# Kernel optimization log

Hardware: AMD Instinct MI355X
Metric: run time of the kernel (lower is better)

## Reference

```python
import jax, jax.numpy as jnp
import numpy as np

ALPHA = 0.2  # LeakyReLU negative slope


def setup_inputs() -> dict:
    key = jax.random.key(0)
    k1, k2, k3 = jax.random.split(key, 3)
    B, N, D_in, D_out = 16, 2048, 128, 128
    x = jax.random.normal(k1, (B, N, D_in), dtype=jnp.float32)
    # xavier-uniform-ish scale for params
    W = jax.random.normal(k2, (D_in, D_out), dtype=jnp.float32) * (1.414 / np.sqrt(D_in + D_out))
    a = jax.random.normal(k3, (2 * D_out, 1), dtype=jnp.float32) * (1.414 / np.sqrt(2 * D_out + 1))
    return {"x": x, "W": W, "a": a}


def reference(x, W, a):
    # h: (B, N, D)
    h = jnp.matmul(x, W)
    D = h.shape[-1]
    # a = [a1; a2]; e[b,i,j] = leakyrelu(a1 . h_i + a2 . h_j)
    a1 = a[:D, 0]   # (D,)
    a2 = a[D:, 0]   # (D,)
    s1 = jnp.einsum('bnd,d->bn', h, a1)  # (B, N) source term
    s2 = jnp.einsum('bnd,d->bn', h, a2)  # (B, N) target term
    e = jax.nn.leaky_relu(s1[:, :, None] + s2[:, None, :], negative_slope=ALPHA)  # (B, N, N)
    attention = jax.nn.softmax(e, axis=2)
    h_prime = jnp.matmul(attention, h)  # (B, N, D)
    return jax.nn.relu(h_prime)  # concat=True -> relu
```

## Files before the change

### kernel.cpp

```cpp
#include <hip/hip_runtime.h>
#include <hip/hip_bf16.h>
#include <cstddef>

#define GAT_B 16
#define GAT_N 2048
#define GAT_D 128
#define GAT_ROWS (GAT_B * GAT_N)
#define CH 256
#define CL 8
#define GAT_ALPHA 0.2f

typedef __attribute__((ext_vector_type(8))) short short8v;
typedef __attribute__((ext_vector_type(4))) float f32x4;

__device__ __forceinline__ void cvt_hilo(float x, unsigned short& hi, unsigned short& lo) {
  union { float f; unsigned u; } a;
  a.f = x;
  hi = (unsigned short)(a.u >> 16);
  union { unsigned u; float f; } b;
  b.u = (unsigned)hi << 16;
  union { float f; unsigned u; } c;
  c.f = x - b.f;
  lo = (unsigned short)(c.u >> 16);
}

__global__ __launch_bounds__(256) void k1_gemm(const float* __restrict__ x,
                                               const float* __restrict__ W,
                                               const float* __restrict__ aa,
                                               float* __restrict__ h,
                                               float* __restrict__ s1part,
                                               float* __restrict__ s2part) {
  __shared__ unsigned short xH[64 * 128];
  __shared__ unsigned short xL[64 * 128];
  const int tid = threadIdx.x;
  const int row0 = blockIdx.x * 64;

#pragma unroll
  for (int p = 0; p < 8; ++p) {
    const int row = p * 8 + (tid >> 5);
    const int f4 = tid & 31;
    const float4 v = ((const float4*)(x + (size_t)(row0 + row) * GAT_D))[f4];
    unsigned short h0, h1, h2, h3, l0, l1, l2, l3;
    cvt_hilo(v.x, h0, l0);
    cvt_hilo(v.y, h1, l1);
    cvt_hilo(v.z, h2, l2);
    cvt_hilo(v.w, h3, l3);
    const int slot = (f4 >> 1) ^ (row & 7);
    const int base = row * 128 + slot * 8 + (f4 & 1) * 4;
    *(ushort4*)&xH[base] = make_ushort4(h0, h1, h2, h3);
    *(ushort4*)&xL[base] = make_ushort4(l0, l1, l2, l3);
  }

  const int w = tid >> 6, l = tid & 63;
  const int wc0 = w * 32;
  const int g = l >> 4, c16 = l & 15;

  short8v bh[4][2], bl[4][2];
#pragma unroll
  for (int ks = 0; ks < 4; ++ks)
#pragma unroll
    for (int nt = 0; nt < 2; ++nt) {
      const int n = wc0 + nt * 16 + c16;
#pragma unroll
      for (int j = 0; j < 8; ++j) {
        unsigned short hi, lo;
        cvt_hilo(W[(ks * 32 + g * 8 + j) * 128 + n], hi, lo);
        bh[ks][nt][j] = (short)hi;
        bl[ks][nt][j] = (short)lo;
      }
    }

  __syncthreads();

  f32x4 acc[4][2];
#pragma unroll
  for (int mt = 0; mt < 4; ++mt)
#pragma unroll
    for (int nt = 0; nt < 2; ++nt) acc[mt][nt] = (f32x4)(0.f);

#pragma unroll
  for (int ks = 0; ks < 4; ++ks) {
    short8v ah[4], al[4];
#pragma unroll
    for (int mt = 0; mt < 4; ++mt) {
      const int row = mt * 16 + c16;
      const int ai = row * 128 + (((ks * 4 + g) ^ (row & 7)) * 8);
      ah[mt] = *(const short8v*)&xH[ai];
      al[mt] = *(const short8v*)&xL[ai];
    }
#pragma unroll
    for (int mt = 0; mt < 4; ++mt) {
#pragma unroll
      for (int nt = 0; nt < 2; ++nt) {
        acc[mt][nt] = __builtin_amdgcn_mfma_f32_16x16x32_bf16(ah[mt], bh[ks][nt], acc[mt][nt], 0, 0, 0);
        acc[mt][nt] = __builtin_amdgcn_mfma_f32_16x16x32_bf16(al[mt], bh[ks][nt], acc[mt][nt], 0, 0, 0);
        acc[mt][nt] = __builtin_amdgcn_mfma_f32_16x16x32_bf16(ah[mt], bl[ks][nt], acc[mt][nt], 0, 0, 0);
      }
    }
  }

#pragma unroll
  for (int mt = 0; mt < 4; ++mt)
#pragma unroll
    for (int nt = 0; nt < 2; ++nt)
#pragma unroll
      for (int j = 0; j < 4; ++j)
        h[(size_t)(row0 + mt * 16 + g * 4 + j) * GAT_D + wc0 + nt * 16 + c16] =
            acc[mt][nt][j];

  float a1v[2], a2v[2];
#pragma unroll
  for (int nt = 0; nt < 2; ++nt) {
    a1v[nt] = aa[wc0 + nt * 16 + c16];
    a2v[nt] = aa[128 + wc0 + nt * 16 + c16];
  }
#pragma unroll
  for (int mt = 0; mt < 4; ++mt) {
#pragma unroll
    for (int j = 0; j < 4; ++j) {
      float t1 = acc[mt][0][j] * a1v[0] + acc[mt][1][j] * a1v[1];
      float t2 = acc[mt][0][j] * a2v[0] + acc[mt][1][j] * a2v[1];
#pragma unroll
      for (int off = 1; off < 16; off <<= 1) {
        t1 += __shfl_xor(t1, off);
        t2 += __shfl_xor(t2, off);
      }
      if (c16 == 0) {
        const int row = row0 + mt * 16 + g * 4 + j;
        s1part[w * GAT_ROWS + row] = t1;
        s2part[w * GAT_ROWS + row] = t2;
      }
    }
  }
}

__global__ __launch_bounds__(1024) void k2_sort(const float* __restrict__ s1part,
                                                const float* __restrict__ s2part,
                                                float* __restrict__ s2s,
                                                int* __restrict__ idxs,
                                                float* __restrict__ s1s,
                                                int* __restrict__ rids,
                                                float* __restrict__ wA,
                                                float* __restrict__ wP,
                                                float* __restrict__ preDenA,
                                                float* __restrict__ sufDenP) {
  __shared__ float v[2048];
  __shared__ int id[2048];
  __shared__ float wtotA[16];
  __shared__ float wtotP[16];
  const int tid = threadIdx.x;
  const int b = blockIdx.x >> 1;
  const int half = blockIdx.x & 1;
  const int i0 = tid, i1 = tid + 1024;
  const float* src = (half == 0) ? s2part : s1part;
  {
    const int r0 = b * GAT_N + i0, r1 = b * GAT_N + i1;
    float v0 = src[r0] + src[GAT_ROWS + r0] + src[2 * GAT_ROWS + r0] + src[3 * GAT_ROWS + r0];
    float v1 = src[r1] + src[GAT_ROWS + r1] + src[2 * GAT_ROWS + r1] + src[3 * GAT_ROWS + r1];
    if (half == 1) {
      v0 = -v0;
      v1 = -v1;
    }
    v[i0] = v0;
    v[i1] = v1;
  }
  __syncthreads();

  const int lane = tid & 63;
  const int e0 = ((tid >> 6) << 7) + lane * 2;
  const int e1 = e0 + 1;
  float va = v[e0], vb = v[e1];
  int ida = e0, idb = e1;

  auto lanex = [&](int k, int j) {
    const int jl = j >> 1;
    const bool dir = (e0 & k) == 0;
    const bool lower = (lane & jl) == 0;
    const bool keepMax = lower ^ dir;
    {
      const float ov = __shfl_xor(va, jl);
      const int oid = __shfl_xor(ida, jl);
      const bool ogt = (ov > va) || (ov == va && oid > ida);
      if (ogt == keepMax) { va = ov; ida = oid; }
    }
    {
      const float ov = __shfl_xor(vb, jl);
      const int oid = __shfl_xor(idb, jl);
      const bool ogt = (ov > vb) || (ov == vb && oid > idb);
      if (ogt == keepMax) { vb = ov; idb = oid; }
    }
  };
  auto pairx = [&](int k) {
    const bool dir = (e0 & k) == 0;
    const bool bgt = (vb > va) || (vb == va && idb > ida);
    if (bgt != dir) {
      const float tv = va; va = vb; vb = tv;
      const int ti = ida; ida = idb; idb = ti;
    }
  };

#pragma unroll
  for (int k = 2; k <= 128; k <<= 1) {
#pragma unroll
    for (int j = k >> 1; j >= 2; j >>= 1) lanex(k, j);
    pairx(k);
  }
  v[e0] = va; id[e0] = ida;
  v[e1] = vb; id[e1] = idb;
  __syncthreads();

  for (int k = 256; k <= 2048; k <<= 1) {
    for (int j = k >> 1; j >= 128; j >>= 1) {
      const int i = ((tid & ~(j - 1)) << 1) | (tid & (j - 1));
      const int ixj = i | j;
      const bool up = (i & k) == 0;
      const float x0 = v[i], x1 = v[ixj];
      if (up ? (x0 > x1) : (x0 < x1)) {
        v[i] = x1;
        v[ixj] = x0;
        const int ti = id[i];
        id[i] = id[ixj];
        id[ixj] = ti;
      }
      __syncthreads();
    }
    va = v[e0]; ida = id[e0];
    vb = v[e1]; idb = id[e1];
#pragma unroll
    for (int j = 64; j >= 2; j >>= 1) lanex(k, j);
    pairx(k);
    v[e0] = va; id[e0] = ida;
    v[e1] = vb; id[e1] = idb;
    __syncthreads();
  }

  if (half == 1) {
    s1s[b * GAT_N + i0] = -v[i0];
    s1s[b * GAT_N + i1] = -v[i1];
    rids[b * GAT_N + i0] = id[i0];
    rids[b * GAT_N + i1] = id[i1];
    return;
  }
  s2s[b * GAT_N + i0] = v[i0];
  s2s[b * GAT_N + i1] = v[i1];
  idxs[b * GAT_N + i0] = id[i0];
  idxs[b * GAT_N + i1] = id[i1];

  const int w = tid >> 6;
  const float aL = __expf(GAT_ALPHA * v[2 * tid]);
  const float aR = __expf(GAT_ALPHA * v[2 * tid + 1]);
  const float pL = __expf(v[2047 - 2 * tid]);
  const float pR = __expf(v[2046 - 2 * tid]);
  wA[b * GAT_N + 2 * tid] = aL;
  wA[b * GAT_N + 2 * tid + 1] = aR;
  wP[b * GAT_N + 2047 - 2 * tid] = pL;
  wP[b * GAT_N + 2046 - 2 * tid] = pR;
  float sA = aL + aR, sP = pL + pR;
#pragma unroll
  for (int off = 1; off < 64; off <<= 1) {
    const float tA = __shfl_up(sA, off);
    const float tP = __shfl_up(sP, off);
    if (lane >= off) {
      sA += tA;
      sP += tP;
    }
  }
  if (lane == 63) {
    wtotA[w] = sA;
    wtotP[w] = sP;
  }
  __syncthreads();
  float offA = 0.f, offP = 0.f;
  for (int ww = 0; ww < w; ++ww) {
    offA += wtotA[ww];
    offP += wtotP[ww];
  }
  const float inclA = offA + sA;
  const float inclP = offP + sP;
  preDenA[b * GAT_N + 2 * tid] = inclA - aR;
  preDenA[b * GAT_N + 2 * tid + 1] = inclA;
  sufDenP[b * GAT_N + 2047 - 2 * tid] = inclP - pR;
  sufDenP[b * GAT_N + 2046 - 2 * tid] = inclP;
}

__global__ __launch_bounds__(128) void k3_permute(const float* __restrict__ h,
                                                  const int* __restrict__ idxs,
                                                  const float* __restrict__ wA,
                                                  const float* __restrict__ wP,
                                                  float* __restrict__ hs,
                                                  float* __restrict__ partA,
                                                  float* __restrict__ partP) {
  const int b = blockIdx.x >> 7, cc = blockIdx.x & 127;
  const int d = threadIdx.x;
  const int* idxb = idxs + b * GAT_N;
  const float* hb = h + (size_t)b * GAT_N * GAT_D;
#pragma unroll
  for (int sub = 0; sub < 2; ++sub) {
    const int c = cc * 2 + sub;
    const int q0 = c * CL;
    float accA = 0.f, accP = 0.f;
#pragma unroll
    for (int qq = 0; qq < CL; ++qq) {
      const int q = q0 + qq;
      const int j = idxb[q];
      const float hv = hb[(size_t)j * GAT_D + d];
      hs[((size_t)b * GAT_N + q) * GAT_D + d] = hv;
      accA = fmaf(wA[b * GAT_N + q], hv, accA);
      accP = fmaf(wP[b * GAT_N + q], hv, accP);
    }
    partA[(b * CH + c) * GAT_D + d] = accA;
    partP[(b * CH + c) * GAT_D + d] = accP;
  }
}

__global__ __launch_bounds__(1024) void k3b_prep(const float* __restrict__ s1s,
                                                 const float* __restrict__ s2s,
                                                 const float* __restrict__ preDenA,
                                                 const float* __restrict__ sufDenP,
                                                 const float* __restrict__ partA,
                                                 const float* __restrict__ partP,
                                                 float* __restrict__ baseA,
                                                 float* __restrict__ baseP,
                                                 int* __restrict__ pArr,
                                                 float* __restrict__ c1,
                                                 float* __restrict__ c2) {
  __shared__ float totA[8][128];
  __shared__ float totP[8][128];
  __shared__ float sh[2048];
  const int b = blockIdx.x >> 1;
  const int role = blockIdx.x & 1;
  const int t = threadIdx.x;
  if (role == 0) {
    const int d = t & 127, g = t >> 7;
    const float* pA = partA + (size_t)(b * CH + g * 32) * GAT_D + d;
    const float* pP = partP + (size_t)(b * CH + g * 32) * GAT_D + d;
    float sA = 0.f, sP = 0.f;
#pragma unroll 8
    for (int i = 0; i < 32; ++i) {
      sA += pA[i * GAT_D];
      sP += pP[i * GAT_D];
    }
    totA[g][d] = sA;
    totP[g][d] = sP;
    __syncthreads();
    float offA = 0.f, offP = 0.f;
    for (int gg = 0; gg < g; ++gg) offA += totA[gg][d];
    for (int gg = g + 1; gg < 8; ++gg) offP += totP[gg][d];
    float run = offA;
#pragma unroll 8
    for (int i = 0; i < 32; ++i) {
      baseA[(size_t)(b * (CH + 1) + g * 32 + i) * GAT_D + d] = run;
      run += pA[i * GAT_D];
    }
    if (g == 7) baseA[(size_t)(b * (CH + 1) + CH) * GAT_D + d] = run;
    run = offP;
#pragma unroll 8
    for (int i = 31; i >= 0; --i) {
      baseP[(size_t)(b * CH + g * 32 + i) * GAT_D + d] = run;
      run += pP[i * GAT_D];
    }
  } else {
    sh[t] = s2s[b * GAT_N + t];
    sh[t + 1024] = s2s[b * GAT_N + t + 1024];
    __syncthreads();
#pragma unroll
    for (int rr = 0; rr < 2; ++rr) {
      const int j = t + rr * 1024;
      const float s1v = s1s[b * GAT_N + j];
      const float tt = -s1v;
      int lo = 0, hi = GAT_N;
      while (lo < hi) {
        const int mid = (lo + hi) >> 1;
        if (sh[mid] < tt)
          lo = mid + 1;
        else
          hi = mid;
      }
      const float e1 = __expf(s1v), e2 = __expf(GAT_ALPHA * s1v);
      float den = 0.f;
      if (lo < GAT_N) den += e1 * sufDenP[b * GAT_N + lo];
      if (lo > 0) den += e2 * preDenA[b * GAT_N + lo - 1];
      const float inv = 1.f / den;
      pArr[b * GAT_N + j] = lo;
      c1[b * GAT_N + j] = e1 * inv;
      c2[b * GAT_N + j] = e2 * inv;
    }
  }
}

__global__ __launch_bounds__(256) void k5_out(const float* __restrict__ hs,
                                              const float* __restrict__ wA,
                                              const float* __restrict__ wP,
                                              const float* __restrict__ baseA,
                                              const float* __restrict__ baseP,
                                              const int* __restrict__ pArr,
                                              const float* __restrict__ c1,
                                              const float* __restrict__ c2,
                                              const int* __restrict__ rids,
                                              float* __restrict__ out) {
  const int wave = threadIdx.x >> 6, lane = threadIdx.x & 63;
  const int j = blockIdx.x * 4 + wave;
  const int b = j >> 11;
  const int jr = b * GAT_N + (j & 2047);
  const int p = pArr[jr];
  const float cc1 = c1[jr], cc2 = c2[jr];
  const int rid = rids[jr];
  const float2* hs2 = (const float2*)(hs + (size_t)b * GAT_N * GAT_D);
  const float* wAb = wA + b * GAT_N;
  const float* wPb = wP + b * GAT_N;

  const int cA = p >> 3;
  float2 accA = ((const float2*)(baseA + (size_t)(b * (CH + 1) + cA) * GAT_D))[lane];
#pragma unroll 4
  for (int q = cA * CL; q < p; ++q) {
    const float w = wAb[q];
    const float2 hv = hs2[(size_t)q * 64 + lane];
    accA.x = fmaf(w, hv.x, accA.x);
    accA.y = fmaf(w, hv.y, accA.y);
  }

  const int pP = p < GAT_N ? p : GAT_N - 1;
  const int cP = pP >> 3;
  float2 accP = ((const float2*)(baseP + (size_t)(b * CH + cP) * GAT_D))[lane];
  const int qend = cP * CL + CL;
#pragma unroll 4
  for (int q = p; q < qend; ++q) {
    const float w = wPb[q];
    const float2 hv = hs2[(size_t)q * 64 + lane];
    accP.x = fmaf(w, hv.x, accP.x);
    accP.y = fmaf(w, hv.y, accP.y);
  }

  const float vx = cc2 * accA.x + cc1 * accP.x;
  const float vy = cc2 * accA.y + cc1 * accP.y;
  ((float2*)out)[(size_t)(b * GAT_N + rid) * 64 + lane] =
      make_float2(fmaxf(vx, 0.f), fmaxf(vy, 0.f));
}

extern "C" void kernel_launch(void* const* d_in, const int* in_sizes, int n_in,
                              void* d_out, int out_size, void* d_ws, size_t ws_size,
                              hipStream_t stream) {
  (void)in_sizes;
  (void)n_in;
  (void)out_size;
  (void)ws_size;
  const float* x = (const float*)d_in[0];
  const float* W = (const float*)d_in[1];
  const float* a = (const float*)d_in[2];
  float* out = (float*)d_out;
  float* wsf = (float*)d_ws;

  const size_t HN = (size_t)GAT_ROWS * GAT_D;
  size_t o = 0;
  float* s1part = wsf + o;   o += 4 * GAT_ROWS;
  float* s2part = wsf + o;   o += 4 * GAT_ROWS;
  float* s2s = wsf + o;      o += GAT_ROWS;
  int* idxs = (int*)(wsf + o); o += GAT_ROWS;
  float* s1s = wsf + o;      o += GAT_ROWS;
  int* rids = (int*)(wsf + o); o += GAT_ROWS;
  float* preDenA = wsf + o;  o += GAT_ROWS;
  float* sufDenP = wsf + o;  o += GAT_ROWS;
  float* wAr = wsf + o;      o += GAT_ROWS;
  float* wPr = wsf + o;      o += GAT_ROWS;
  int* pArr = (int*)(wsf + o); o += GAT_ROWS;
  float* c1 = wsf + o;       o += GAT_ROWS;
  float* c2 = wsf + o;       o += GAT_ROWS;
  float* partA = wsf + o;    o += (size_t)GAT_B * CH * GAT_D;
  float* partP = wsf + o;    o += (size_t)GAT_B * CH * GAT_D;
  float* baseA = wsf + o;    o += (size_t)GAT_B * (CH + 1) * GAT_D;
  float* baseP = wsf + o;    o += (size_t)GAT_B * CH * GAT_D;
  float* h = wsf + o;        o += HN;
  float* hs = wsf + o;       o += HN;

  k1_gemm<<<512, 256, 0, stream>>>(x, W, a, h, s1part, s2part);
  k2_sort<<<2 * GAT_B, 1024, 0, stream>>>(s1part, s2part, s2s, idxs, s1s, rids, wAr, wPr,
                                          preDenA, sufDenP);
  k3_permute<<<GAT_B * 128, 128, 0, stream>>>(h, idxs, wAr, wPr, hs, partA, partP);
  k3b_prep<<<2 * GAT_B, 1024, 0, stream>>>(s1s, s2s, preDenA, sufDenP, partA, partP,
                                           baseA, baseP, pArr, c1, c2);
  k5_out<<<GAT_ROWS / 4, 256, 0, stream>>>(hs, wAr, wPr, baseA, baseP, pArr, c1, c2,
                                           rids, out);
}
```

Before: 66.35 us.

## Move binary search and softmax coefficients into sort kernel, slim scan kernel

The per-row binary search and softmax-denominator coefficient computation move from the prep kernel into the s2-sort block. That block now keeps prefix/suffix denominators in shared memory and indexes results by natural row id instead of sorted order. The prep kernel is reduced to the partial-sum scan over half as many blocks. Several intermediate global arrays (s1s, s2s, preDenA, sufDenP) go away. The output kernel now gathers p/c1/c2 through rids and uses 512-thread blocks, while the sort block takes on extra serial work.

```diff
diff --git a/kernel.cpp b/kernel.cpp
--- a/kernel.cpp
+++ b/kernel.cpp
@@ -136,16 +136,17 @@
 
 __global__ __launch_bounds__(1024) void k2_sort(const float* __restrict__ s1part,
                                                 const float* __restrict__ s2part,
-                                                float* __restrict__ s2s,
                                                 int* __restrict__ idxs,
-                                                float* __restrict__ s1s,
                                                 int* __restrict__ rids,
                                                 float* __restrict__ wA,
                                                 float* __restrict__ wP,
-                                                float* __restrict__ preDenA,
-                                                float* __restrict__ sufDenP) {
+                                                int* __restrict__ pNat,
+                                                float* __restrict__ c1,
+                                                float* __restrict__ c2) {
   __shared__ float v[2048];
   __shared__ int id[2048];
+  __shared__ float denA[2048];
+  __shared__ float denP[2048];
   __shared__ float wtotA[16];
   __shared__ float wtotP[16];
   const int tid = threadIdx.x;
@@ -235,14 +236,10 @@
   }
 
   if (half == 1) {
-    s1s[b * GAT_N + i0] = -v[i0];
-    s1s[b * GAT_N + i1] = -v[i1];
     rids[b * GAT_N + i0] = id[i0];
     rids[b * GAT_N + i1] = id[i1];
     return;
   }
-  s2s[b * GAT_N + i0] = v[i0];
-  s2s[b * GAT_N + i1] = v[i1];
   idxs[b * GAT_N + i0] = id[i0];
   idxs[b * GAT_N + i1] = id[i1];
 
@@ -277,10 +274,36 @@
   }
   const float inclA = offA + sA;
   const float inclP = offP + sP;
-  preDenA[b * GAT_N + 2 * tid] = inclA - aR;
-  preDenA[b * GAT_N + 2 * tid + 1] = inclA;
-  sufDenP[b * GAT_N + 2047 - 2 * tid] = inclP - pR;
-  sufDenP[b * GAT_N + 2046 - 2 * tid] = inclP;
+  denA[2 * tid] = inclA - aR;
+  denA[2 * tid + 1] = inclA;
+  denP[2047 - 2 * tid] = inclP - pR;
+  denP[2046 - 2 * tid] = inclP;
+  __syncthreads();
+
+#pragma unroll
+  for (int rr = 0; rr < 2; ++rr) {
+    const int j = tid + rr * 1024;
+    const int r = b * GAT_N + j;
+    const float s1v = s1part[r] + s1part[GAT_ROWS + r] + s1part[2 * GAT_ROWS + r] +
+                      s1part[3 * GAT_ROWS + r];
+    const float tt = -s1v;
+    int lo = 0, hi = GAT_N;
+    while (lo < hi) {
+      const int mid = (lo + hi) >> 1;
+      if (v[mid] < tt)
+        lo = mid + 1;
+      else
+        hi = mid;
+    }
+    const float e1 = __expf(s1v), e2 = __expf(GAT_ALPHA * s1v);
+    float den = 0.f;
+    if (lo < GAT_N) den += e1 * denP[lo];
+    if (lo > 0) den += e2 * denA[lo - 1];
+    const float inv = 1.f / den;
+    pNat[r] = lo;
+    c1[r] = e1 * inv;
+    c2[r] = e2 * inv;
+  }
 }
 
 __global__ __launch_bounds__(128) void k3_permute(const float* __restrict__ h,
@@ -313,98 +336,62 @@
   }
 }
 
-__global__ __launch_bounds__(1024) void k3b_prep(const float* __restrict__ s1s,
-                                                 const float* __restrict__ s2s,
-                                                 const float* __restrict__ preDenA,
-                                                 const float* __restrict__ sufDenP,
-                                                 const float* __restrict__ partA,
+__global__ __launch_bounds__(1024) void k3b_scan(const float* __restrict__ partA,
                                                  const float* __restrict__ partP,
                                                  float* __restrict__ baseA,
-                                                 float* __restrict__ baseP,
-                                                 int* __restrict__ pArr,
-                                                 float* __restrict__ c1,
-                                                 float* __restrict__ c2) {
+                                                 float* __restrict__ baseP) {
   __shared__ float totA[8][128];
   __shared__ float totP[8][128];
-  __shared__ float sh[2048];
-  const int b = blockIdx.x >> 1;
-  const int role = blockIdx.x & 1;
+  const int b = blockIdx.x;
   const int t = threadIdx.x;
-  if (role == 0) {
-    const int d = t & 127, g = t >> 7;
-    const float* pA = partA + (size_t)(b * CH + g * 32) * GAT_D + d;
-    const float* pP = partP + (size_t)(b * CH + g * 32) * GAT_D + d;
-    float sA = 0.f, sP = 0.f;
+  const int d = t & 127, g = t >> 7;
+  const float* pA = partA + (size_t)(b * CH + g * 32) * GAT_D + d;
+  const float* pP = partP + (size_t)(b * CH + g * 32) * GAT_D + d;
+  float sA = 0.f, sP = 0.f;
 #pragma unroll 8
-    for (int i = 0; i < 32; ++i) {
-      sA += pA[i * GAT_D];
-      sP += pP[i * GAT_D];
-    }
-    totA[g][d] = sA;
-    totP[g][d] = sP;
-    __syncthreads();
-    float offA = 0.f, offP = 0.f;
-    for (int gg = 0; gg < g; ++gg) offA += totA[gg][d];
-    for (int gg = g + 1; gg < 8; ++gg) offP += totP[gg][d];
-    float run = offA;
+  for (int i = 0; i < 32; ++i) {
+    sA += pA[i * GAT_D];
+    sP += pP[i * GAT_D];
+  }
+  totA[g][d] = sA;
+  totP[g][d] = sP;
+  __syncthreads();
+  float offA = 0.f, offP = 0.f;
+  for (int gg = 0; gg < g; ++gg) offA += totA[gg][d];
+  for (int gg = g + 1; gg < 8; ++gg) offP += totP[gg][d];
+  float run = offA;
 #pragma unroll 8
-    for (int i = 0; i < 32; ++i) {
-      baseA[(size_t)(b * (CH + 1) + g * 32 + i) * GAT_D + d] = run;
-      run += pA[i * GAT_D];
-    }
-    if (g == 7) baseA[(size_t)(b * (CH + 1) + CH) * GAT_D + d] = run;
-    run = offP;
+  for (int i = 0; i < 32; ++i) {
+    baseA[(size_t)(b * (CH + 1) + g * 32 + i) * GAT_D + d] = run;
+    run += pA[i * GAT_D];
+  }
+  if (g == 7) baseA[(size_t)(b * (CH + 1) + CH) * GAT_D + d] = run;
+  run = offP;
 #pragma unroll 8
-    for (int i = 31; i >= 0; --i) {
-      baseP[(size_t)(b * CH + g * 32 + i) * GAT_D + d] = run;
-      run += pP[i * GAT_D];
-    }
-  } else {
-    sh[t] = s2s[b * GAT_N + t];
-    sh[t + 1024] = s2s[b * GAT_N + t + 1024];
-    __syncthreads();
-#pragma unroll
-    for (int rr = 0; rr < 2; ++rr) {
-      const int j = t + rr * 1024;
-      const float s1v = s1s[b * GAT_N + j];
-      const float tt = -s1v;
-      int lo = 0, hi = GAT_N;
-      while (lo < hi) {
-        const int mid = (lo + hi) >> 1;
-        if (sh[mid] < tt)
-          lo = mid + 1;
-        else
-          hi = mid;
-      }
-      const float e1 = __expf(s1v), e2 = __expf(GAT_ALPHA * s1v);
-      float den = 0.f;
-      if (lo < GAT_N) den += e1 * sufDenP[b * GAT_N + lo];
-      if (lo > 0) den += e2 * preDenA[b * GAT_N + lo - 1];
-      const float inv = 1.f / den;
-      pArr[b * GAT_N + j] = lo;
-      c1[b * GAT_N + j] = e1 * inv;
-      c2[b * GAT_N + j] = e2 * inv;
-    }
-  }
-}
-
-__global__ __launch_bounds__(256) void k5_out(const float* __restrict__ hs,
+  for (int i = 31; i >= 0; --i) {
+    baseP[(size_t)(b * CH + g * 32 + i) * GAT_D + d] = run;
+    run += pP[i * GAT_D];
+  }
+}
+
+__global__ __launch_bounds__(512) void k5_out(const float* __restrict__ hs,
                                               const float* __restrict__ wA,
                                               const float* __restrict__ wP,
                                               const float* __restrict__ baseA,
                                               const float* __restrict__ baseP,
-                                              const int* __restrict__ pArr,
+                                              const int* __restrict__ pNat,
                                               const float* __restrict__ c1,
                                               const float* __restrict__ c2,
                                               const int* __restrict__ rids,
                                               float* __restrict__ out) {
   const int wave = threadIdx.x >> 6, lane = threadIdx.x & 63;
-  const int j = blockIdx.x * 4 + wave;
+  const int j = blockIdx.x * 8 + wave;
   const int b = j >> 11;
   const int jr = b * GAT_N + (j & 2047);
-  const int p = pArr[jr];
-  const float cc1 = c1[jr], cc2 = c2[jr];
   const int rid = rids[jr];
+  const int nr = b * GAT_N + rid;
+  const int p = pNat[nr];
+  const float cc1 = c1[nr], cc2 = c2[nr];
   const float2* hs2 = (const float2*)(hs + (size_t)b * GAT_N * GAT_D);
   const float* wAb = wA + b * GAT_N;
   const float* wPb = wP + b * GAT_N;
@@ -433,7 +420,7 @@
 
   const float vx = cc2 * accA.x + cc1 * accP.x;
   const float vy = cc2 * accA.y + cc1 * accP.y;
-  ((float2*)out)[(size_t)(b * GAT_N + rid) * 64 + lane] =
+  ((float2*)out)[(size_t)nr * 64 + lane] =
       make_float2(fmaxf(vx, 0.f), fmaxf(vy, 0.f));
 }
 
@@ -454,15 +441,11 @@
   size_t o = 0;
   float* s1part = wsf + o;   o += 4 * GAT_ROWS;
   float* s2part = wsf + o;   o += 4 * GAT_ROWS;
-  float* s2s = wsf + o;      o += GAT_ROWS;
   int* idxs = (int*)(wsf + o); o += GAT_ROWS;
-  float* s1s = wsf + o;      o += GAT_ROWS;
   int* rids = (int*)(wsf + o); o += GAT_ROWS;
-  float* preDenA = wsf + o;  o += GAT_ROWS;
-  float* sufDenP = wsf + o;  o += GAT_ROWS;
   float* wAr = wsf + o;      o += GAT_ROWS;
   float* wPr = wsf + o;      o += GAT_ROWS;
-  int* pArr = (int*)(wsf + o); o += GAT_ROWS;
+  int* pNat = (int*)(wsf + o); o += GAT_ROWS;
   float* c1 = wsf + o;       o += GAT_ROWS;
   float* c2 = wsf + o;       o += GAT_ROWS;
   float* partA = wsf + o;    o += (size_t)GAT_B * CH * GAT_D;
@@ -473,11 +456,10 @@
   float* hs = wsf + o;       o += HN;
 
   k1_gemm<<<512, 256, 0, stream>>>(x, W, a, h, s1part, s2part);
-  k2_sort<<<2 * GAT_B, 1024, 0, stream>>>(s1part, s2part, s2s, idxs, s1s, rids, wAr, wPr,
-                                          preDenA, sufDenP);
+  k2_sort<<<2 * GAT_B, 1024, 0, stream>>>(s1part, s2part, idxs, rids, wAr, wPr,
+                                          pNat, c1, c2);
   k3_permute<<<GAT_B * 128, 128, 0, stream>>>(h, idxs, wAr, wPr, hs, partA, partP);
-  k3b_prep<<<2 * GAT_B, 1024, 0, stream>>>(s1s, s2s, preDenA, sufDenP, partA, partP,
-                                           baseA, baseP, pArr, c1, c2);
-  k5_out<<<GAT_ROWS / 4, 256, 0, stream>>>(hs, wAr, wPr, baseA, baseP, pArr, c1, c2,
+  k3b_scan<<<GAT_B, 1024, 0, stream>>>(partA, partP, baseA, baseP);
+  k5_out<<<GAT_ROWS / 8, 512, 0, stream>>>(hs, wAr, wPr, baseA, baseP, pNat, c1, c2,
                                            rids, out);
 }
```

Result: slower. 71.31 us (+7.5%).
